# Kernel tuning notes

Measured on AMD Instinct MI355X. Metric: run time of the kernel, lower is better.

Reference implementation:

```python
import jax, jax.numpy as jnp
import numpy as np

N = 16384   # flat token count
D = 256     # d_model
M = 64      # median_size (attention in_features / hidden_features)
OUT = 1     # output_size


def setup_inputs() -> dict:
    key = jax.random.key(0)
    ks = jax.random.split(key, 12)
    sD = 1.0 / np.sqrt(D)
    sM = 1.0 / np.sqrt(M)
    rn = lambda k, shape, s: (jax.random.normal(k, shape, jnp.float32) * s)
    return {
        "x":    rn(ks[0], (N, D), 1.0),
        "W1":   rn(ks[1], (D, M), sD), "b1": jnp.zeros((M,), jnp.float32),
        # 3 stacked attention blocks
        "Wq":   rn(ks[2], (3, M, M), sM), "bq": jnp.zeros((3, M), jnp.float32),
        "Wk":   rn(ks[3], (3, M, M), sM), "bk": jnp.zeros((3, M), jnp.float32),
        "Wv":   rn(ks[4], (3, M, M), sM), "bv": jnp.zeros((3, M), jnp.float32),
        "Wf1":  rn(ks[5], (3, M, M), sM), "bf1": jnp.zeros((3, M), jnp.float32),
        "Wf2":  rn(ks[6], (3, M, M), sM), "bf2": jnp.zeros((3, M), jnp.float32),
        "ln_g": jnp.ones((3, M), jnp.float32), "ln_b": jnp.zeros((3, M), jnp.float32),
        "Wout": rn(ks[7], (M, OUT), sM), "bout": jnp.zeros((OUT,), jnp.float32),
    }


def leaky(x, slope):
    return jnp.where(x >= 0, x, slope * x)


def layer_norm(x, g, b, eps=1e-5):
    mu = jnp.mean(x, axis=-1, keepdims=True)
    var = jnp.mean((x - mu) ** 2, axis=-1, keepdims=True)
    return (x - mu) * jax.lax.rsqrt(var + eps) * g + b


def attn_block(x, Wq, bq, Wk, bk, Wv, bv, Wf1, bf1, Wf2, bf2):
    # per-token outer-product attention: attn[n] = softmax(q[n] k[n]^T) over last dim
    q = x @ Wq + bq            # [N, M]
    k = x @ Wk + bk
    v = x @ Wv + bv
    a = jax.nn.softmax(q[:, :, None] * k[:, None, :], axis=-1)   # [N, M, M]
    y = jnp.einsum('nij,nj->ni', a, v) + x                       # residual add (x += x0)
    h = leaky(y @ Wf1 + bf1, 0.01)                               # LeakyReLU(0.01)
    h = h @ Wf2 + bf2
    return h + y                                                 # pred=False residual


def reference(x, W1, b1, Wq, bq, Wk, bk, Wv, bv, Wf1, bf1, Wf2, bf2, ln_g, ln_b, Wout, bout):
    h = x @ W1 + b1                 # Linear_1
    res = leaky(h, 0.1)             # x1 = LeakyReLU(0.1)(h)
    cur = h                         # transformer_1 is applied to pre-activation h
    for t in range(3):
        a = attn_block(cur, Wq[t], bq[t], Wk[t], bk[t], Wv[t], bv[t],
                       Wf1[t], bf1[t], Wf2[t], bf2[t])
        a = layer_norm(a, ln_g[t], ln_b[t])
        res = a + res               # x2 = LN(...) + x1, etc.
        cur = res
    out = leaky(res @ Wout + bout, 0.1).reshape(-1, OUT)
    return (out, out, out, out, out)
```

## Files before the change

kernel.cpp:

```cpp
#include <hip/hip_runtime.h>

#define NTOK 16384
#define TB 8

typedef float f32x4_t __attribute__((ext_vector_type(4)));
typedef short s16x8_t __attribute__((ext_vector_type(8)));

union bfpack { unsigned int u[4]; s16x8_t v; };

__device__ __forceinline__ unsigned int pk2bf(float lo, float hi) {
    unsigned int r;
    asm("v_cvt_pk_bf16_f32 %0, %1, %2" : "=v"(r) : "v"(lo), "v"(hi));
    return r;
}
__device__ __forceinline__ unsigned short f2bf(float f) {
    unsigned int r;
    asm("v_cvt_pk_bf16_f32 %0, %1, %1" : "=v"(r) : "v"(f));
    return (unsigned short)r;
}
__device__ __forceinline__ unsigned short f2bf_host_style(float f) {
    unsigned int x = __float_as_uint(f);
    x += 0x7fffu + ((x >> 16) & 1u);
    return (unsigned short)(x >> 16);
}
__device__ __forceinline__ float fexp2(float x) {
#if __has_builtin(__builtin_amdgcn_exp2f)
    return __builtin_amdgcn_exp2f(x);
#else
    return exp2f(x);
#endif
}
__device__ __forceinline__ float frcp(float x) {
#if __has_builtin(__builtin_amdgcn_rcpf)
    return __builtin_amdgcn_rcpf(x);
#else
    return 1.0f / x;
#endif
}
__device__ __forceinline__ float frsq(float x) {
#if __has_builtin(__builtin_amdgcn_rsqf)
    return __builtin_amdgcn_rsqf(x);
#else
    return rsqrtf(x);
#endif
}

__global__ __launch_bounds__(256)
void prep_kernel(const float* __restrict__ W1,
                 const float* __restrict__ Wq, const float* __restrict__ Wk,
                 const float* __restrict__ Wv, const float* __restrict__ Wf1,
                 const float* __restrict__ Wf2, unsigned short* __restrict__ wsb)
{
    const int i = blockIdx.x * 256 + threadIdx.x;
    if (i < 16384) {
        const int m = i >> 8, k = i & 255;
        wsb[i] = f2bf_host_style(W1[k * 64 + m]);
    } else if (i < 77824) {
        const int u  = i - 16384;
        const int mi = u >> 12;
        const int st = mi / 5, q = mi % 5;
        const int r  = u & 4095;
        const int hk = r >> 11;
        const int r1 = r & 2047;
        const int w  = r1 >> 9;
        const int r2 = r1 & 511;
        const int l  = r2 >> 3;
        const int e  = r2 & 7;
        const int m  = w * 16 + (l & 15);
        const int k  = hk * 32 + (l >> 4) * 8 + e;
        const float* src = q == 0 ? Wq : q == 1 ? Wk : q == 2 ? Wv : q == 3 ? Wf1 : Wf2;
        wsb[i] = f2bf_host_style(src[st * 4096 + k * 64 + m]);
    }
}

__global__ __launch_bounds__(256, 4)
void tf3_kernel(const float* __restrict__ x,
                const float* __restrict__ b1,
                const float* __restrict__ bq, const float* __restrict__ bk,
                const float* __restrict__ bv,
                const float* __restrict__ bf1, const float* __restrict__ bf2,
                const float* __restrict__ lng, const float* __restrict__ lnb,
                const float* __restrict__ Wout, const float* __restrict__ bout,
                const unsigned short* __restrict__ wsb,
                float* __restrict__ out)
{
    __shared__ __align__(16) char smem[15104];
    unsigned short* a_lds = (unsigned short*)smem;
    float* q_lds  = (float*)(smem + 2048);
    float* ky_lds = (float*)(smem + 6400);
    float* v_lds  = (float*)(smem + 10752);
    char*  x_img  = smem + 2048;

    const int tid = threadIdx.x;
    const int wv  = tid >> 6;
    const int l   = tid & 63;
    const int n0  = blockIdx.x * TB;

    const int lr  = l & 15;
    const int q4  = l >> 4;
    const int c   = wv * 16 + lr;

    const int e2 = l & 31;
    const int th = wv * 2 + (l >> 5);

    float res_reg[2], cur_reg[2];

    auto LOADM = [&](int mat, s16x8_t& r0, s16x8_t& r1) {
        const char* gb = (const char*)(wsb + 16384 + mat * 4096) + wv * 1024 + l * 16;
        r0 = *reinterpret_cast<const s16x8_t*>(gb);
        r1 = *reinterpret_cast<const s16x8_t*>(gb + 4096);
    };
    auto mmd = [&](s16x8_t af0, s16x8_t af1, s16x8_t b0, s16x8_t b1) -> f32x4_t {
        f32x4_t acc = __builtin_amdgcn_mfma_f32_16x16x32_bf16(af0, b0, (f32x4_t){0.f,0.f,0.f,0.f}, 0, 0, 0);
        acc = __builtin_amdgcn_mfma_f32_16x16x32_bf16(af1, b1, acc, 0, 0, 0);
        return acc;
    };

    s16x8_t bq0, bq1, bk0, bk1, bv0, bv1;
    s16x8_t f10, f11;
    s16x8_t f20, f21;

    LOADM(0, bq0, bq1); LOADM(1, bk0, bk1); LOADM(2, bv0, bv1);

    {
        const int r  = tid >> 5;
        const int cc = tid & 31;
        const float* xp = x + (size_t)(n0 + r) * 256 + cc * 8;
        const float4 u0 = *reinterpret_cast<const float4*>(xp);
        const float4 u1 = *reinterpret_cast<const float4*>(xp + 4);
        bfpack P;
        P.u[0] = pk2bf(u0.x, u0.y); P.u[1] = pk2bf(u0.z, u0.w);
        P.u[2] = pk2bf(u1.x, u1.y); P.u[3] = pk2bf(u1.z, u1.w);
        *reinterpret_cast<s16x8_t*>(x_img + r * 512 + ((cc ^ (r & 7)) << 4)) = P.v;
    }
    __syncthreads();

    f32x4_t acch = {0.f, 0.f, 0.f, 0.f};
    #pragma unroll
    for (int s5 = 0; s5 < 8; ++s5) {
        const s16x8_t af = *reinterpret_cast<const s16x8_t*>(
            x_img + lr * 512 + (((s5 * 4 + q4) ^ (lr & 7)) << 4));
        const s16x8_t bf = *reinterpret_cast<const s16x8_t*>(&wsb[c * 256 + s5 * 32 + q4 * 8]);
        acch = __builtin_amdgcn_mfma_f32_16x16x32_bf16(af, bf, acch, 0, 0, 0);
    }
    __syncthreads();
    {
        const float bb = b1[c];
        #pragma unroll
        for (int rg = 0; rg < 4; ++rg)
            q_lds[(q4 * 4 + rg) * 68 + c] = acch[rg] + bb;
    }
    __syncthreads();
    #pragma unroll
    for (int tt = 0; tt < 2; ++tt) {
        const int t = wv * 2 + tt;
        const float h = q_lds[t * 68 + l];
        cur_reg[tt] = h;
        res_reg[tt] = h >= 0.f ? h : 0.1f * h;
        a_lds[t * 64 + (((l >> 3) ^ (t & 7)) * 8) + (l & 7)] = f2bf(h);
    }

    for (int st = 0; st < 3; ++st) {
        const float bqv  = bq[st * 64 + c];
        const float bkv  = bk[st * 64 + c];
        const float bvv  = bv[st * 64 + c];
        const float bf1v = bf1[st * 64 + c];
        const float bf2v = bf2[st * 64 + c];
        const float lngv = lng[st * 64 + l];
        const float lnbv = lnb[st * 64 + l];

        __syncthreads();
        {
            const s16x8_t af0 = *reinterpret_cast<const s16x8_t*>(&a_lds[lr * 64 + ((q4       ^ (lr & 7)) * 8)]);
            const s16x8_t af1 = *reinterpret_cast<const s16x8_t*>(&a_lds[lr * 64 + (((4 + q4) ^ (lr & 7)) * 8)]);
            f32x4_t aq = mmd(af0, af1, bq0, bq1);
            f32x4_t ak = mmd(af0, af1, bk0, bk1);
            f32x4_t av = mmd(af0, af1, bv0, bv1);
            #pragma unroll
            for (int rg = 0; rg < 4; ++rg) {
                const int tr = q4 * 4 + rg;
                q_lds[tr * 68 + c]  = aq[rg] + bqv;
                ky_lds[tr * 68 + c] = ak[rg] + bkv;
                v_lds[tr * 68 + c]  = av[rg] + bvv;
            }
        }
        LOADM(st * 5 + 3, f10, f11);
        __syncthreads();

        float kmax_t[2], kmin_t[2];
        {
            const float2 kv = *reinterpret_cast<const float2*>(&ky_lds[th * 68 + e2 * 2]);
            float kmx = fmaxf(kv.x, kv.y);
            float kmn = fminf(kv.x, kv.y);
            #pragma unroll
            for (int m = 1; m < 32; m <<= 1) {
                kmx = fmaxf(kmx, __shfl_xor(kmx, m, 64));
                kmn = fminf(kmn, __shfl_xor(kmn, m, 64));
            }
            #pragma unroll
            for (int tt = 0; tt < 2; ++tt) {
                kmax_t[tt] = __shfl(kmx, tt * 32, 64);
                kmin_t[tt] = __shfl(kmn, tt * 32, 64);
            }
        }
        #pragma unroll
        for (int tt = 0; tt < 2; ++tt) {
            const int t = wv * 2 + tt;
            const float qs = q_lds[t * 68 + l] * 1.44269504088896340736f;
            const float m2 = fmaxf(qs * kmax_t[tt], qs * kmin_t[tt]);
            const float* kb = &ky_lds[t * 68];
            const float* vb = &v_lds[t * 68];
            float s0 = 0.f, s1 = 0.f, p0 = 0.f, p1 = 0.f;
            #pragma unroll
            for (int j = 0; j < 64; j += 4) {
                const float4 kj = *reinterpret_cast<const float4*>(kb + j);
                const float4 vj = *reinterpret_cast<const float4*>(vb + j);
                const float e0 = fexp2(fmaf(qs, kj.x, -m2)); s0 += e0; p0 = fmaf(e0, vj.x, p0);
                const float e1 = fexp2(fmaf(qs, kj.y, -m2)); s1 += e1; p1 = fmaf(e1, vj.y, p1);
                const float e2v = fexp2(fmaf(qs, kj.z, -m2)); s0 += e2v; p0 = fmaf(e2v, vj.z, p0);
                const float e3 = fexp2(fmaf(qs, kj.w, -m2)); s1 += e3; p1 = fmaf(e3, vj.w, p1);
            }
            const float y = (p0 + p1) * frcp(s0 + s1) + cur_reg[tt];
            ky_lds[t * 68 + l] = y;
        }
        LOADM(st * 5 + 4, f20, f21);
        __syncthreads();

        {
            f32x4_t acc = {0.f, 0.f, 0.f, 0.f};
            #pragma unroll
            for (int kh = 0; kh < 2; ++kh) {
                const float* yp = &ky_lds[lr * 68 + kh * 32 + q4 * 8];
                const float4 y0 = *reinterpret_cast<const float4*>(yp);
                const float4 y1 = *reinterpret_cast<const float4*>(yp + 4);
                bfpack P;
                P.u[0] = pk2bf(y0.x, y0.y); P.u[1] = pk2bf(y0.z, y0.w);
                P.u[2] = pk2bf(y1.x, y1.y); P.u[3] = pk2bf(y1.z, y1.w);
                acc = __builtin_amdgcn_mfma_f32_16x16x32_bf16(P.v, kh ? f11 : f10, acc, 0, 0, 0);
            }
            #pragma unroll
            for (int rg = 0; rg < 4; ++rg) {
                const int tr = q4 * 4 + rg;
                float h = acc[rg] + bf1v;
                h = h >= 0.f ? h : 0.01f * h;
                a_lds[tr * 64 + (((c >> 3) ^ (tr & 7)) * 8) + (c & 7)] = f2bf(h);
            }
        }
        __syncthreads();

        {
            const s16x8_t ag0 = *reinterpret_cast<const s16x8_t*>(&a_lds[lr * 64 + ((q4       ^ (lr & 7)) * 8)]);
            const s16x8_t ag1 = *reinterpret_cast<const s16x8_t*>(&a_lds[lr * 64 + (((4 + q4) ^ (lr & 7)) * 8)]);
            f32x4_t acc = mmd(ag0, ag1, f20, f21);
            #pragma unroll
            for (int rg = 0; rg < 4; ++rg) {
                const int tr = q4 * 4 + rg;
                ky_lds[tr * 68 + c] += acc[rg] + bf2v;
            }
        }
        __syncthreads();

        if (st < 2) {
            LOADM((st + 1) * 5 + 0, bq0, bq1);
            LOADM((st + 1) * 5 + 1, bk0, bk1);
            LOADM((st + 1) * 5 + 2, bv0, bv1);
        }
        {
            const float2 av2 = *reinterpret_cast<const float2*>(&ky_lds[th * 68 + e2 * 2]);
            float ssum = av2.x + av2.y;
            #pragma unroll
            for (int m = 1; m < 32; m <<= 1) ssum += __shfl_xor(ssum, m, 64);
            const float mug = ssum * 0.015625f;
            const float d0 = av2.x - mug, d1 = av2.y - mug;
            float vsum = d0 * d0 + d1 * d1;
            #pragma unroll
            for (int m = 1; m < 32; m <<= 1) vsum += __shfl_xor(vsum, m, 64);
            #pragma unroll
            for (int tt = 0; tt < 2; ++tt) {
                const int t = wv * 2 + tt;
                const float mu = __shfl(mug, tt * 32, 64);
                const float vv = __shfl(vsum, tt * 32, 64);
                const float rs = frsq(vv * 0.015625f + 1e-5f);
                const float a  = ky_lds[t * 68 + l];
                const float an = (a - mu) * rs * lngv + lnbv;
                const float rnew = res_reg[tt] + an;
                res_reg[tt] = rnew;
                cur_reg[tt] = rnew;
                a_lds[t * 64 + (((l >> 3) ^ (t & 7)) * 8) + (l & 7)] = f2bf(rnew);
            }
        }
    }

    const float wo = Wout[l];
    const float bo = bout[0];
    #pragma unroll
    for (int tt = 0; tt < 2; ++tt)
        q_lds[(wv * 2 + tt) * 68 + l] = res_reg[tt] * wo;
    {
        const float2 pv = *reinterpret_cast<const float2*>(&q_lds[th * 68 + e2 * 2]);
        float p = pv.x + pv.y;
        #pragma unroll
        for (int m = 1; m < 32; m <<= 1) p += __shfl_xor(p, m, 64);
        if (e2 == 0) {
            float o = p + bo;
            o = o >= 0.f ? o : 0.1f * o;
            #pragma unroll
            for (int c5 = 0; c5 < 5; ++c5)
                out[(size_t)c5 * NTOK + n0 + th] = o;
        }
    }
}

extern "C" void kernel_launch(void* const* d_in, const int* in_sizes, int n_in,
                              void* d_out, int out_size, void* d_ws, size_t ws_size,
                              hipStream_t stream) {
    const float* x    = (const float*)d_in[0];
    const float* W1   = (const float*)d_in[1];
    const float* b1   = (const float*)d_in[2];
    const float* Wq   = (const float*)d_in[3];
    const float* bq   = (const float*)d_in[4];
    const float* Wk   = (const float*)d_in[5];
    const float* bk   = (const float*)d_in[6];
    const float* Wv   = (const float*)d_in[7];
    const float* bv   = (const float*)d_in[8];
    const float* Wf1  = (const float*)d_in[9];
    const float* bf1  = (const float*)d_in[10];
    const float* Wf2  = (const float*)d_in[11];
    const float* bf2  = (const float*)d_in[12];
    const float* lngp = (const float*)d_in[13];
    const float* lnbp = (const float*)d_in[14];
    const float* Wout = (const float*)d_in[15];
    const float* bout = (const float*)d_in[16];
    float* outp = (float*)d_out;
    unsigned short* wsb = (unsigned short*)d_ws;

    hipLaunchKernelGGL(prep_kernel, dim3(304), dim3(256), 0, stream,
                       W1, Wq, Wk, Wv, Wf1, Wf2, wsb);
    hipLaunchKernelGGL(tf3_kernel, dim3(NTOK / TB), dim3(256), 0, stream,
                       x, b1, bq, bk, bv, bf1, bf2, lngp, lnbp, Wout, bout,
                       (const unsigned short*)wsb, outp);
}
```

Before: 54.79 us.

## Compute FFN per wave for its own tokens to drop block barriers

The two FFN matmuls in each attention block are restructured. Each wave now computes all 64 output columns for only the two tokens it owns, using four MFMA tiles per K-half instead of one column tile shared across waves. Because each wave only reads and writes its own rows in LDS, three __syncthreads per stage are removed, and the hidden activations move through q_lds in fp32. The cost is about four times as many MFMAs, most of whose output rows are discarded, plus loading the full FFN weight matrices into every wave.

```diff
diff --git a/kernel.cpp b/kernel.cpp
--- a/kernel.cpp
+++ b/kernel.cpp
@@ -110,6 +110,13 @@
         r0 = *reinterpret_cast<const s16x8_t*>(gb);
         r1 = *reinterpret_cast<const s16x8_t*>(gb + 4096);
     };
+    auto LDB4 = [&](int mat, int kh, s16x8_t b[4]) {
+        const char* gb = (const char*)(wsb + 16384) + mat * 8192 + kh * 4096 + l * 16;
+        b[0] = *reinterpret_cast<const s16x8_t*>(gb);
+        b[1] = *reinterpret_cast<const s16x8_t*>(gb + 1024);
+        b[2] = *reinterpret_cast<const s16x8_t*>(gb + 2048);
+        b[3] = *reinterpret_cast<const s16x8_t*>(gb + 3072);
+    };
     auto mmd = [&](s16x8_t af0, s16x8_t af1, s16x8_t b0, s16x8_t b1) -> f32x4_t {
         f32x4_t acc = __builtin_amdgcn_mfma_f32_16x16x32_bf16(af0, b0, (f32x4_t){0.f,0.f,0.f,0.f}, 0, 0, 0);
         acc = __builtin_amdgcn_mfma_f32_16x16x32_bf16(af1, b1, acc, 0, 0, 0);
@@ -117,8 +124,6 @@
     };
 
     s16x8_t bq0, bq1, bk0, bk1, bv0, bv1;
-    s16x8_t f10, f11;
-    s16x8_t f20, f21;
 
     LOADM(0, bq0, bq1); LOADM(1, bk0, bk1); LOADM(2, bv0, bv1);
 
@@ -164,10 +169,14 @@
         const float bqv  = bq[st * 64 + c];
         const float bkv  = bk[st * 64 + c];
         const float bvv  = bv[st * 64 + c];
-        const float bf1v = bf1[st * 64 + c];
-        const float bf2v = bf2[st * 64 + c];
         const float lngv = lng[st * 64 + l];
         const float lnbv = lnb[st * 64 + l];
+        float bf1v4[4], bf2v4[4];
+        #pragma unroll
+        for (int tile = 0; tile < 4; ++tile) {
+            bf1v4[tile] = bf1[st * 64 + tile * 16 + lr];
+            bf2v4[tile] = bf2[st * 64 + tile * 16 + lr];
+        }
 
         __syncthreads();
         {
@@ -184,7 +193,6 @@
                 v_lds[tr * 68 + c]  = av[rg] + bvv;
             }
         }
-        LOADM(st * 5 + 3, f10, f11);
         __syncthreads();
 
         float kmax_t[2], kmin_t[2];
@@ -223,48 +231,79 @@
             const float y = (p0 + p1) * frcp(s0 + s1) + cur_reg[tt];
             ky_lds[t * 68 + l] = y;
         }
-        LOADM(st * 5 + 4, f20, f21);
-        __syncthreads();
-
-        {
-            f32x4_t acc = {0.f, 0.f, 0.f, 0.f};
+
+        {
+            s16x8_t fb0[4], fb1[4];
+            LDB4(st * 5 + 3, 0, fb0);
+            LDB4(st * 5 + 3, 1, fb1);
+            const int arow = (wv * 2 + lr) & 15;
+            f32x4_t ac0 = {0,0,0,0}, ac1 = {0,0,0,0}, ac2 = {0,0,0,0}, ac3 = {0,0,0,0};
             #pragma unroll
             for (int kh = 0; kh < 2; ++kh) {
-                const float* yp = &ky_lds[lr * 68 + kh * 32 + q4 * 8];
+                const float* yp = &ky_lds[arow * 68 + kh * 32 + q4 * 8];
                 const float4 y0 = *reinterpret_cast<const float4*>(yp);
                 const float4 y1 = *reinterpret_cast<const float4*>(yp + 4);
                 bfpack P;
                 P.u[0] = pk2bf(y0.x, y0.y); P.u[1] = pk2bf(y0.z, y0.w);
                 P.u[2] = pk2bf(y1.x, y1.y); P.u[3] = pk2bf(y1.z, y1.w);
-                acc = __builtin_amdgcn_mfma_f32_16x16x32_bf16(P.v, kh ? f11 : f10, acc, 0, 0, 0);
-            }
-            #pragma unroll
-            for (int rg = 0; rg < 4; ++rg) {
-                const int tr = q4 * 4 + rg;
-                float h = acc[rg] + bf1v;
-                h = h >= 0.f ? h : 0.01f * h;
-                a_lds[tr * 64 + (((c >> 3) ^ (tr & 7)) * 8) + (c & 7)] = f2bf(h);
-            }
-        }
-        __syncthreads();
-
-        {
-            const s16x8_t ag0 = *reinterpret_cast<const s16x8_t*>(&a_lds[lr * 64 + ((q4       ^ (lr & 7)) * 8)]);
-            const s16x8_t ag1 = *reinterpret_cast<const s16x8_t*>(&a_lds[lr * 64 + (((4 + q4) ^ (lr & 7)) * 8)]);
-            f32x4_t acc = mmd(ag0, ag1, f20, f21);
-            #pragma unroll
-            for (int rg = 0; rg < 4; ++rg) {
-                const int tr = q4 * 4 + rg;
-                ky_lds[tr * 68 + c] += acc[rg] + bf2v;
-            }
-        }
-        __syncthreads();
+                ac0 = __builtin_amdgcn_mfma_f32_16x16x32_bf16(P.v, kh ? fb1[0] : fb0[0], ac0, 0, 0, 0);
+                ac1 = __builtin_amdgcn_mfma_f32_16x16x32_bf16(P.v, kh ? fb1[1] : fb0[1], ac1, 0, 0, 0);
+                ac2 = __builtin_amdgcn_mfma_f32_16x16x32_bf16(P.v, kh ? fb1[2] : fb0[2], ac2, 0, 0, 0);
+                ac3 = __builtin_amdgcn_mfma_f32_16x16x32_bf16(P.v, kh ? fb1[3] : fb0[3], ac3, 0, 0, 0);
+            }
+            if (q4 == 0) {
+                #pragma unroll
+                for (int rg = 0; rg < 2; ++rg) {
+                    float h0 = ac0[rg] + bf1v4[0]; h0 = h0 >= 0.f ? h0 : 0.01f * h0;
+                    float h1 = ac1[rg] + bf1v4[1]; h1 = h1 >= 0.f ? h1 : 0.01f * h1;
+                    float h2 = ac2[rg] + bf1v4[2]; h2 = h2 >= 0.f ? h2 : 0.01f * h2;
+                    float h3 = ac3[rg] + bf1v4[3]; h3 = h3 >= 0.f ? h3 : 0.01f * h3;
+                    float* qrow = q_lds + (wv * 2 + rg) * 68;
+                    qrow[lr]      = h0;
+                    qrow[16 + lr] = h1;
+                    qrow[32 + lr] = h2;
+                    qrow[48 + lr] = h3;
+                }
+            }
+        }
+
+        {
+            s16x8_t fb0[4], fb1[4];
+            LDB4(st * 5 + 4, 0, fb0);
+            LDB4(st * 5 + 4, 1, fb1);
+            const int arow = (wv * 2 + lr) & 15;
+            f32x4_t ac0 = {0,0,0,0}, ac1 = {0,0,0,0}, ac2 = {0,0,0,0}, ac3 = {0,0,0,0};
+            #pragma unroll
+            for (int kh = 0; kh < 2; ++kh) {
+                const float* hp = &q_lds[arow * 68 + kh * 32 + q4 * 8];
+                const float4 h0 = *reinterpret_cast<const float4*>(hp);
+                const float4 h1 = *reinterpret_cast<const float4*>(hp + 4);
+                bfpack P;
+                P.u[0] = pk2bf(h0.x, h0.y); P.u[1] = pk2bf(h0.z, h0.w);
+                P.u[2] = pk2bf(h1.x, h1.y); P.u[3] = pk2bf(h1.z, h1.w);
+                ac0 = __builtin_amdgcn_mfma_f32_16x16x32_bf16(P.v, kh ? fb1[0] : fb0[0], ac0, 0, 0, 0);
+                ac1 = __builtin_amdgcn_mfma_f32_16x16x32_bf16(P.v, kh ? fb1[1] : fb0[1], ac1, 0, 0, 0);
+                ac2 = __builtin_amdgcn_mfma_f32_16x16x32_bf16(P.v, kh ? fb1[2] : fb0[2], ac2, 0, 0, 0);
+                ac3 = __builtin_amdgcn_mfma_f32_16x16x32_bf16(P.v, kh ? fb1[3] : fb0[3], ac3, 0, 0, 0);
+            }
+            if (q4 == 0) {
+                #pragma unroll
+                for (int rg = 0; rg < 2; ++rg) {
+                    float* krow = ky_lds + (wv * 2 + rg) * 68;
+                    krow[lr]      += ac0[rg] + bf2v4[0];
+                    krow[16 + lr] += ac1[rg] + bf2v4[1];
+                    krow[32 + lr] += ac2[rg] + bf2v4[2];
+                    krow[48 + lr] += ac3[rg] + bf2v4[3];
+                }
+            }
+        }
 
         if (st < 2) {
             LOADM((st + 1) * 5 + 0, bq0, bq1);
             LOADM((st + 1) * 5 + 1, bk0, bk1);
             LOADM((st + 1) * 5 + 2, bv0, bv1);
         }
+
         {
             const float2 av2 = *reinterpret_cast<const float2*>(&ky_lds[th * 68 + e2 * 2]);
             float ssum = av2.x + av2.y;
```

New measurement: 57.95 us. 5.8% more time.

## Process two 8-token groups per block with interleaved stage pipeline

Applied to the files above, without the earlier changes.

Each block now handles 16 tokens as two independent 8-token groups with separate shared-memory buffers. The QKV, attention, FFN and LayerNorm stages of the two groups are staggered so one group's MFMA work sits between the same barriers as the other group's softmax and VALU work. The aim is to hide barrier and latency stalls and to share each weight load and barrier across twice as many tokens. In exchange, shared memory per block doubles, register pressure rises, and the grid has half as many blocks.

```diff
diff --git a/kernel.cpp b/kernel.cpp
--- a/kernel.cpp
+++ b/kernel.cpp
@@ -1,7 +1,6 @@
 #include <hip/hip_runtime.h>
 
 #define NTOK 16384
-#define TB 8
 
 typedef float f32x4_t __attribute__((ext_vector_type(4)));
 typedef short s16x8_t __attribute__((ext_vector_type(8)));
@@ -84,26 +83,30 @@
                 const unsigned short* __restrict__ wsb,
                 float* __restrict__ out)
 {
-    __shared__ __align__(16) char smem[15104];
-    unsigned short* a_lds = (unsigned short*)smem;
-    float* q_lds  = (float*)(smem + 2048);
-    float* ky_lds = (float*)(smem + 6400);
-    float* v_lds  = (float*)(smem + 10752);
-    char*  x_img  = smem + 2048;
+    __shared__ __align__(16) char smem[30208];
+    unsigned short* aA = (unsigned short*)smem;
+    float* qA  = (float*)(smem + 2048);
+    float* kyA = (float*)(smem + 6400);
+    float* vA  = (float*)(smem + 10752);
+    char*  xA  = smem + 2048;
+    unsigned short* aB = (unsigned short*)(smem + 15104);
+    float* qB  = (float*)(smem + 17152);
+    float* kyB = (float*)(smem + 21504);
+    float* vB  = (float*)(smem + 25856);
+    char*  xB  = smem + 17152;
 
     const int tid = threadIdx.x;
     const int wv  = tid >> 6;
     const int l   = tid & 63;
-    const int n0  = blockIdx.x * TB;
+    const int n0  = blockIdx.x * 16;
 
     const int lr  = l & 15;
     const int q4  = l >> 4;
     const int c   = wv * 16 + lr;
-
-    const int e2 = l & 31;
-    const int th = wv * 2 + (l >> 5);
-
-    float res_reg[2], cur_reg[2];
+    const int e2  = l & 31;
+    const int th  = wv * 2 + (l >> 5);
+
+    float resA[2], curA[2], resB[2], curB[2];
 
     auto LOADM = [&](int mat, s16x8_t& r0, s16x8_t& r1) {
         const char* gb = (const char*)(wsb + 16384 + mat * 4096) + wv * 1024 + l * 16;
@@ -117,79 +120,27 @@
     };
 
     s16x8_t bq0, bq1, bk0, bk1, bv0, bv1;
-    s16x8_t f10, f11;
-    s16x8_t f20, f21;
-
-    LOADM(0, bq0, bq1); LOADM(1, bk0, bk1); LOADM(2, bv0, bv1);
-
-    {
-        const int r  = tid >> 5;
-        const int cc = tid & 31;
-        const float* xp = x + (size_t)(n0 + r) * 256 + cc * 8;
-        const float4 u0 = *reinterpret_cast<const float4*>(xp);
-        const float4 u1 = *reinterpret_cast<const float4*>(xp + 4);
-        bfpack P;
-        P.u[0] = pk2bf(u0.x, u0.y); P.u[1] = pk2bf(u0.z, u0.w);
-        P.u[2] = pk2bf(u1.x, u1.y); P.u[3] = pk2bf(u1.z, u1.w);
-        *reinterpret_cast<s16x8_t*>(x_img + r * 512 + ((cc ^ (r & 7)) << 4)) = P.v;
-    }
-    __syncthreads();
-
-    f32x4_t acch = {0.f, 0.f, 0.f, 0.f};
-    #pragma unroll
-    for (int s5 = 0; s5 < 8; ++s5) {
-        const s16x8_t af = *reinterpret_cast<const s16x8_t*>(
-            x_img + lr * 512 + (((s5 * 4 + q4) ^ (lr & 7)) << 4));
-        const s16x8_t bf = *reinterpret_cast<const s16x8_t*>(&wsb[c * 256 + s5 * 32 + q4 * 8]);
-        acch = __builtin_amdgcn_mfma_f32_16x16x32_bf16(af, bf, acch, 0, 0, 0);
-    }
-    __syncthreads();
-    {
-        const float bb = b1[c];
-        #pragma unroll
-        for (int rg = 0; rg < 4; ++rg)
-            q_lds[(q4 * 4 + rg) * 68 + c] = acch[rg] + bb;
-    }
-    __syncthreads();
-    #pragma unroll
-    for (int tt = 0; tt < 2; ++tt) {
-        const int t = wv * 2 + tt;
-        const float h = q_lds[t * 68 + l];
-        cur_reg[tt] = h;
-        res_reg[tt] = h >= 0.f ? h : 0.1f * h;
-        a_lds[t * 64 + (((l >> 3) ^ (t & 7)) * 8) + (l & 7)] = f2bf(h);
-    }
-
-    for (int st = 0; st < 3; ++st) {
-        const float bqv  = bq[st * 64 + c];
-        const float bkv  = bk[st * 64 + c];
-        const float bvv  = bv[st * 64 + c];
-        const float bf1v = bf1[st * 64 + c];
-        const float bf2v = bf2[st * 64 + c];
-        const float lngv = lng[st * 64 + l];
-        const float lnbv = lnb[st * 64 + l];
-
-        __syncthreads();
-        {
-            const s16x8_t af0 = *reinterpret_cast<const s16x8_t*>(&a_lds[lr * 64 + ((q4       ^ (lr & 7)) * 8)]);
-            const s16x8_t af1 = *reinterpret_cast<const s16x8_t*>(&a_lds[lr * 64 + (((4 + q4) ^ (lr & 7)) * 8)]);
-            f32x4_t aq = mmd(af0, af1, bq0, bq1);
-            f32x4_t ak = mmd(af0, af1, bk0, bk1);
-            f32x4_t av = mmd(af0, af1, bv0, bv1);
-            #pragma unroll
-            for (int rg = 0; rg < 4; ++rg) {
-                const int tr = q4 * 4 + rg;
-                q_lds[tr * 68 + c]  = aq[rg] + bqv;
-                ky_lds[tr * 68 + c] = ak[rg] + bkv;
-                v_lds[tr * 68 + c]  = av[rg] + bvv;
-            }
-        }
-        LOADM(st * 5 + 3, f10, f11);
-        __syncthreads();
-
+    s16x8_t f10, f11, f20, f21;
+
+    auto QKVp = [&](unsigned short* ag, float* qg, float* kyg, float* vg,
+                    float bqv, float bkv, float bvv) {
+        const s16x8_t af0 = *reinterpret_cast<const s16x8_t*>(&ag[lr * 64 + ((q4       ^ (lr & 7)) * 8)]);
+        const s16x8_t af1 = *reinterpret_cast<const s16x8_t*>(&ag[lr * 64 + (((4 + q4) ^ (lr & 7)) * 8)]);
+        f32x4_t aq = mmd(af0, af1, bq0, bq1);
+        f32x4_t ak = mmd(af0, af1, bk0, bk1);
+        f32x4_t av = mmd(af0, af1, bv0, bv1);
+        #pragma unroll
+        for (int rg = 0; rg < 4; ++rg) {
+            const int tr = q4 * 4 + rg;
+            qg[tr * 68 + c]  = aq[rg] + bqv;
+            kyg[tr * 68 + c] = ak[rg] + bkv;
+            vg[tr * 68 + c]  = av[rg] + bvv;
+        }
+    };
+    auto ATTp = [&](float* qg, float* kyg, float* vg, float (&cur)[2]) {
         float kmax_t[2], kmin_t[2];
         {
-            const float2 kv = *reinterpret_cast<const float2*>(&ky_lds[th * 68 + e2 * 2]);
+            const float2 kv = *reinterpret_cast<const float2*>(&kyg[th * 68 + e2 * 2]);
             float kmx = fmaxf(kv.x, kv.y);
             float kmn = fminf(kv.x, kv.y);
             #pragma unroll
@@ -206,10 +157,10 @@
         #pragma unroll
         for (int tt = 0; tt < 2; ++tt) {
             const int t = wv * 2 + tt;
-            const float qs = q_lds[t * 68 + l] * 1.44269504088896340736f;
+            const float qs = qg[t * 68 + l] * 1.44269504088896340736f;
             const float m2 = fmaxf(qs * kmax_t[tt], qs * kmin_t[tt]);
-            const float* kb = &ky_lds[t * 68];
-            const float* vb = &v_lds[t * 68];
+            const float* kb = &kyg[t * 68];
+            const float* vb = &vg[t * 68];
             float s0 = 0.f, s1 = 0.f, p0 = 0.f, p1 = 0.f;
             #pragma unroll
             for (int j = 0; j < 64; j += 4) {
@@ -220,84 +171,72 @@
                 const float e2v = fexp2(fmaf(qs, kj.z, -m2)); s0 += e2v; p0 = fmaf(e2v, vj.z, p0);
                 const float e3 = fexp2(fmaf(qs, kj.w, -m2)); s1 += e3; p1 = fmaf(e3, vj.w, p1);
             }
-            const float y = (p0 + p1) * frcp(s0 + s1) + cur_reg[tt];
-            ky_lds[t * 68 + l] = y;
-        }
-        LOADM(st * 5 + 4, f20, f21);
-        __syncthreads();
-
-        {
-            f32x4_t acc = {0.f, 0.f, 0.f, 0.f};
-            #pragma unroll
-            for (int kh = 0; kh < 2; ++kh) {
-                const float* yp = &ky_lds[lr * 68 + kh * 32 + q4 * 8];
-                const float4 y0 = *reinterpret_cast<const float4*>(yp);
-                const float4 y1 = *reinterpret_cast<const float4*>(yp + 4);
-                bfpack P;
-                P.u[0] = pk2bf(y0.x, y0.y); P.u[1] = pk2bf(y0.z, y0.w);
-                P.u[2] = pk2bf(y1.x, y1.y); P.u[3] = pk2bf(y1.z, y1.w);
-                acc = __builtin_amdgcn_mfma_f32_16x16x32_bf16(P.v, kh ? f11 : f10, acc, 0, 0, 0);
-            }
-            #pragma unroll
-            for (int rg = 0; rg < 4; ++rg) {
-                const int tr = q4 * 4 + rg;
-                float h = acc[rg] + bf1v;
-                h = h >= 0.f ? h : 0.01f * h;
-                a_lds[tr * 64 + (((c >> 3) ^ (tr & 7)) * 8) + (c & 7)] = f2bf(h);
-            }
-        }
-        __syncthreads();
-
-        {
-            const s16x8_t ag0 = *reinterpret_cast<const s16x8_t*>(&a_lds[lr * 64 + ((q4       ^ (lr & 7)) * 8)]);
-            const s16x8_t ag1 = *reinterpret_cast<const s16x8_t*>(&a_lds[lr * 64 + (((4 + q4) ^ (lr & 7)) * 8)]);
-            f32x4_t acc = mmd(ag0, ag1, f20, f21);
-            #pragma unroll
-            for (int rg = 0; rg < 4; ++rg) {
-                const int tr = q4 * 4 + rg;
-                ky_lds[tr * 68 + c] += acc[rg] + bf2v;
-            }
-        }
-        __syncthreads();
-
-        if (st < 2) {
-            LOADM((st + 1) * 5 + 0, bq0, bq1);
-            LOADM((st + 1) * 5 + 1, bk0, bk1);
-            LOADM((st + 1) * 5 + 2, bv0, bv1);
-        }
-        {
-            const float2 av2 = *reinterpret_cast<const float2*>(&ky_lds[th * 68 + e2 * 2]);
-            float ssum = av2.x + av2.y;
-            #pragma unroll
-            for (int m = 1; m < 32; m <<= 1) ssum += __shfl_xor(ssum, m, 64);
-            const float mug = ssum * 0.015625f;
-            const float d0 = av2.x - mug, d1 = av2.y - mug;
-            float vsum = d0 * d0 + d1 * d1;
-            #pragma unroll
-            for (int m = 1; m < 32; m <<= 1) vsum += __shfl_xor(vsum, m, 64);
-            #pragma unroll
-            for (int tt = 0; tt < 2; ++tt) {
-                const int t = wv * 2 + tt;
-                const float mu = __shfl(mug, tt * 32, 64);
-                const float vv = __shfl(vsum, tt * 32, 64);
-                const float rs = frsq(vv * 0.015625f + 1e-5f);
-                const float a  = ky_lds[t * 68 + l];
-                const float an = (a - mu) * rs * lngv + lnbv;
-                const float rnew = res_reg[tt] + an;
-                res_reg[tt] = rnew;
-                cur_reg[tt] = rnew;
-                a_lds[t * 64 + (((l >> 3) ^ (t & 7)) * 8) + (l & 7)] = f2bf(rnew);
-            }
-        }
-    }
-
-    const float wo = Wout[l];
-    const float bo = bout[0];
-    #pragma unroll
-    for (int tt = 0; tt < 2; ++tt)
-        q_lds[(wv * 2 + tt) * 68 + l] = res_reg[tt] * wo;
-    {
-        const float2 pv = *reinterpret_cast<const float2*>(&q_lds[th * 68 + e2 * 2]);
+            const float y = (p0 + p1) * frcp(s0 + s1) + cur[tt];
+            kyg[t * 68 + l] = y;
+        }
+    };
+    auto F1p = [&](float* kyg, unsigned short* ag, float bf1v) {
+        f32x4_t acc = {0.f, 0.f, 0.f, 0.f};
+        #pragma unroll
+        for (int kh = 0; kh < 2; ++kh) {
+            const float* yp = &kyg[lr * 68 + kh * 32 + q4 * 8];
+            const float4 y0 = *reinterpret_cast<const float4*>(yp);
+            const float4 y1 = *reinterpret_cast<const float4*>(yp + 4);
+            bfpack P;
+            P.u[0] = pk2bf(y0.x, y0.y); P.u[1] = pk2bf(y0.z, y0.w);
+            P.u[2] = pk2bf(y1.x, y1.y); P.u[3] = pk2bf(y1.z, y1.w);
+            acc = __builtin_amdgcn_mfma_f32_16x16x32_bf16(P.v, kh ? f11 : f10, acc, 0, 0, 0);
+        }
+        #pragma unroll
+        for (int rg = 0; rg < 4; ++rg) {
+            const int tr = q4 * 4 + rg;
+            float h = acc[rg] + bf1v;
+            h = h >= 0.f ? h : 0.01f * h;
+            ag[tr * 64 + (((c >> 3) ^ (tr & 7)) * 8) + (c & 7)] = f2bf(h);
+        }
+    };
+    auto F2p = [&](unsigned short* ag, float* kyg, float bf2v) {
+        const s16x8_t ag0 = *reinterpret_cast<const s16x8_t*>(&ag[lr * 64 + ((q4       ^ (lr & 7)) * 8)]);
+        const s16x8_t ag1 = *reinterpret_cast<const s16x8_t*>(&ag[lr * 64 + (((4 + q4) ^ (lr & 7)) * 8)]);
+        f32x4_t acc = mmd(ag0, ag1, f20, f21);
+        #pragma unroll
+        for (int rg = 0; rg < 4; ++rg) {
+            const int tr = q4 * 4 + rg;
+            kyg[tr * 68 + c] += acc[rg] + bf2v;
+        }
+    };
+    auto LNp = [&](float* kyg, unsigned short* ag, float (&cur)[2], float (&res)[2],
+                   float lngv, float lnbv) {
+        const float2 av2 = *reinterpret_cast<const float2*>(&kyg[th * 68 + e2 * 2]);
+        float ssum = av2.x + av2.y;
+        #pragma unroll
+        for (int m = 1; m < 32; m <<= 1) ssum += __shfl_xor(ssum, m, 64);
+        const float mug = ssum * 0.015625f;
+        const float d0 = av2.x - mug, d1 = av2.y - mug;
+        float vsum = d0 * d0 + d1 * d1;
+        #pragma unroll
+        for (int m = 1; m < 32; m <<= 1) vsum += __shfl_xor(vsum, m, 64);
+        #pragma unroll
+        for (int tt = 0; tt < 2; ++tt) {
+            const int t = wv * 2 + tt;
+            const float mu = __shfl(mug, tt * 32, 64);
+            const float vv = __shfl(vsum, tt * 32, 64);
+            const float rs = frsq(vv * 0.015625f + 1e-5f);
+            const float a  = kyg[t * 68 + l];
+            const float an = (a - mu) * rs * lngv + lnbv;
+            const float rnew = res[tt] + an;
+            res[tt] = rnew;
+            cur[tt] = rnew;
+            ag[t * 64 + (((l >> 3) ^ (t & 7)) * 8) + (l & 7)] = f2bf(rnew);
+        }
+    };
+    auto HEADp = [&](float* qg, float (&res)[2], int base) {
+        const float wo = Wout[l];
+        const float bo = bout[0];
+        #pragma unroll
+        for (int tt = 0; tt < 2; ++tt)
+            qg[(wv * 2 + tt) * 68 + l] = res[tt] * wo;
+        const float2 pv = *reinterpret_cast<const float2*>(&qg[th * 68 + e2 * 2]);
         float p = pv.x + pv.y;
         #pragma unroll
         for (int m = 1; m < 32; m <<= 1) p += __shfl_xor(p, m, 64);
@@ -306,9 +245,103 @@
             o = o >= 0.f ? o : 0.1f * o;
             #pragma unroll
             for (int c5 = 0; c5 < 5; ++c5)
-                out[(size_t)c5 * NTOK + n0 + th] = o;
-        }
-    }
+                out[(size_t)c5 * NTOK + base + th] = o;
+        }
+    };
+
+    LOADM(0, bq0, bq1); LOADM(1, bk0, bk1); LOADM(2, bv0, bv1);
+
+    {
+        const int r  = tid >> 5;
+        const int cc = tid & 31;
+        const float* xpA = x + (size_t)(n0 + r) * 256 + cc * 8;
+        const float* xpB = x + (size_t)(n0 + 8 + r) * 256 + cc * 8;
+        const float4 a0 = *reinterpret_cast<const float4*>(xpA);
+        const float4 a1 = *reinterpret_cast<const float4*>(xpA + 4);
+        const float4 b0 = *reinterpret_cast<const float4*>(xpB);
+        const float4 b1v = *reinterpret_cast<const float4*>(xpB + 4);
+        bfpack PA, PB;
+        PA.u[0] = pk2bf(a0.x, a0.y); PA.u[1] = pk2bf(a0.z, a0.w);
+        PA.u[2] = pk2bf(a1.x, a1.y); PA.u[3] = pk2bf(a1.z, a1.w);
+        PB.u[0] = pk2bf(b0.x, b0.y); PB.u[1] = pk2bf(b0.z, b0.w);
+        PB.u[2] = pk2bf(b1v.x, b1v.y); PB.u[3] = pk2bf(b1v.z, b1v.w);
+        const int off = r * 512 + ((cc ^ (r & 7)) << 4);
+        *reinterpret_cast<s16x8_t*>(xA + off) = PA.v;
+        *reinterpret_cast<s16x8_t*>(xB + off) = PB.v;
+    }
+    __syncthreads();
+
+    f32x4_t accA = {0.f,0.f,0.f,0.f}, accB = {0.f,0.f,0.f,0.f};
+    #pragma unroll
+    for (int s5 = 0; s5 < 8; ++s5) {
+        const s16x8_t bf = *reinterpret_cast<const s16x8_t*>(&wsb[c * 256 + s5 * 32 + q4 * 8]);
+        const int off = lr * 512 + (((s5 * 4 + q4) ^ (lr & 7)) << 4);
+        const s16x8_t afA = *reinterpret_cast<const s16x8_t*>(xA + off);
+        const s16x8_t afB = *reinterpret_cast<const s16x8_t*>(xB + off);
+        accA = __builtin_amdgcn_mfma_f32_16x16x32_bf16(afA, bf, accA, 0, 0, 0);
+        accB = __builtin_amdgcn_mfma_f32_16x16x32_bf16(afB, bf, accB, 0, 0, 0);
+    }
+    __syncthreads();
+    {
+        const float bb = b1[c];
+        #pragma unroll
+        for (int rg = 0; rg < 4; ++rg) {
+            const int tr = q4 * 4 + rg;
+            qA[tr * 68 + c] = accA[rg] + bb;
+            qB[tr * 68 + c] = accB[rg] + bb;
+        }
+    }
+    __syncthreads();
+    #pragma unroll
+    for (int tt = 0; tt < 2; ++tt) {
+        const int t = wv * 2 + tt;
+        const float hA = qA[t * 68 + l];
+        curA[tt] = hA;
+        resA[tt] = hA >= 0.f ? hA : 0.1f * hA;
+        aA[t * 64 + (((l >> 3) ^ (t & 7)) * 8) + (l & 7)] = f2bf(hA);
+        const float hB = qB[t * 68 + l];
+        curB[tt] = hB;
+        resB[tt] = hB >= 0.f ? hB : 0.1f * hB;
+        aB[t * 64 + (((l >> 3) ^ (t & 7)) * 8) + (l & 7)] = f2bf(hB);
+    }
+
+    for (int st = 0; st < 3; ++st) {
+        const float bqv  = bq[st * 64 + c];
+        const float bkv  = bk[st * 64 + c];
+        const float bvv  = bv[st * 64 + c];
+        const float bf1v = bf1[st * 64 + c];
+        const float bf2v = bf2[st * 64 + c];
+        const float lngv = lng[st * 64 + l];
+        const float lnbv = lnb[st * 64 + l];
+
+        __syncthreads();
+        if (st > 0)
+            LNp(kyB, aB, curB, resB, lng[(st - 1) * 64 + l], lnb[(st - 1) * 64 + l]);
+        QKVp(aA, qA, kyA, vA, bqv, bkv, bvv);
+        __syncthreads();
+        LOADM(st * 5 + 3, f10, f11);
+        QKVp(aB, qB, kyB, vB, bqv, bkv, bvv);
+        ATTp(qA, kyA, vA, curA);
+        __syncthreads();
+        LOADM(st * 5 + 4, f20, f21);
+        F1p(kyA, aA, bf1v);
+        ATTp(qB, kyB, vB, curB);
+        __syncthreads();
+        if (st < 2) {
+            LOADM((st + 1) * 5 + 0, bq0, bq1);
+            LOADM((st + 1) * 5 + 1, bk0, bk1);
+            LOADM((st + 1) * 5 + 2, bv0, bv1);
+        }
+        F2p(aA, kyA, bf2v);
+        F1p(kyB, aB, bf1v);
+        __syncthreads();
+        F2p(aB, kyB, bf2v);
+        LNp(kyA, aA, curA, resA, lngv, lnbv);
+    }
+    __syncthreads();
+    LNp(kyB, aB, curB, resB, lng[2 * 64 + l], lnb[2 * 64 + l]);
+    HEADp(qA, resA, n0);
+    HEADp(qB, resB, n0 + 8);
 }
 
 extern "C" void kernel_launch(void* const* d_in, const int* in_sizes, int n_in,
@@ -336,7 +369,7 @@
 
     hipLaunchKernelGGL(prep_kernel, dim3(304), dim3(256), 0, stream,
                        W1, Wq, Wk, Wv, Wf1, Wf2, wsb);
-    hipLaunchKernelGGL(tf3_kernel, dim3(NTOK / TB), dim3(256), 0, stream,
+    hipLaunchKernelGGL(tf3_kernel, dim3(NTOK / 16), dim3(256), 0, stream,
                        x, b1, bq, bk, bv, bf1, bf2, lngp, lnbp, Wout, bout,
                        (const unsigned short*)wsb, outp);
 }
```

Result: slower. 56.38 us (+2.9%).
